# Kernel optimization log

Hardware: AMD Instinct MI355X
Metric: run time of the kernel (lower is better)

## Reference

```python
import jax, jax.numpy as jnp
import numpy as np

N = 50000      # nodes
E = 800000     # edges (avg degree 16)
D_IN = 64
D_H = 64


def setup_inputs() -> dict:
    key = jax.random.key(0)
    k = jax.random.split(key, 4)
    x = jax.random.normal(k[0], (N, D_IN), dtype=jnp.float32)
    edge_index = jax.random.randint(k[1], (2, E), 0, N, dtype=jnp.int64)
    W1 = jax.random.normal(k[2], (D_IN, D_H), dtype=jnp.float32) * (1.0 / np.sqrt(D_IN))
    b1 = jnp.zeros((D_H,), dtype=jnp.float32)
    W2 = jax.random.normal(k[3], (D_H, 1), dtype=jnp.float32) * (1.0 / np.sqrt(D_H))
    b2 = jnp.zeros((1,), dtype=jnp.float32)
    return {"x": x, "edge_index": edge_index, "W1": W1, "b1": b1, "W2": W2, "b2": b2}


def gcn_conv(x, src, dst, W, b):
    """PyG-style GCNConv: linear -> symmetric-normalized scatter-aggregate + bias.
    src/dst already include self-loops."""
    n = x.shape[0]
    h = x @ W                                                   # [N, Dout]
    deg = jax.ops.segment_sum(jnp.ones_like(dst, dtype=h.dtype), dst, num_segments=n)
    dinv_sqrt = jnp.where(deg > 0, jax.lax.rsqrt(jnp.maximum(deg, 1e-12)), 0.0)
    norm = dinv_sqrt[src] * dinv_sqrt[dst]                       # [E+N]
    agg = jax.ops.segment_sum(h[src] * norm[:, None], dst, num_segments=n)
    return agg + b


def reference(x, edge_index, W1, b1, W2, b2):
    n = x.shape[0]
    loops = jnp.arange(n, dtype=edge_index.dtype)
    src = jnp.concatenate([edge_index[0], loops])                # add self-loops
    dst = jnp.concatenate([edge_index[1], loops])
    h = jax.nn.relu(gcn_conv(x, src, dst, W1, b1))               # [N, D_H]
    out = gcn_conv(h, src, dst, W2, b2)                          # [N, 1]
    return out.squeeze(-1)                                       # [N]
```

## Files before the change

kernel.cpp:

```cpp
#include <hip/hip_runtime.h>

#define D 64
#define PW2 256
#define PSH2 8
#define EPB 4096

__global__ __launch_bounds__(256) void k_hist(const int* __restrict__ dst, int E,
                                              int* __restrict__ counts, int NP) {
    extern __shared__ int lh[];
    int t = threadIdx.x, b = blockIdx.x;
    for (int i = t; i < NP; i += 256) lh[i] = 0;
    __syncthreads();
    int base = b * EPB;
#pragma unroll
    for (int k = 0; k < EPB / 256; ++k) {
        int e = base + k * 256 + t;
        if (e < E) atomicAdd(&lh[dst[e] >> PSH2], 1);
    }
    __syncthreads();
    for (int i = t; i < NP; i += 256) counts[(size_t)b * NP + i] = lh[i];
}

__global__ __launch_bounds__(256) void k_scanA(int* __restrict__ counts, int NB, int NP,
                                               int* __restrict__ bin_total) {
    __shared__ int sh[256];
    int t = threadIdx.x, bin = blockIdx.x;
    int v = (t < NB) ? counts[(size_t)t * NP + bin] : 0;
    sh[t] = v;
    __syncthreads();
    for (int off = 1; off < 256; off <<= 1) {
        int u = (t >= off) ? sh[t - off] : 0;
        __syncthreads();
        sh[t] += u;
        __syncthreads();
    }
    if (t < NB) counts[(size_t)t * NP + bin] = sh[t] - v;
    if (t == 255) bin_total[bin] = sh[255];
}

__global__ __launch_bounds__(256) void k_scanB(const int* __restrict__ bin_total, int NP,
                                               int* __restrict__ bin_base) {
    __shared__ int sh[256];
    int t = threadIdx.x;
    int v = (t < NP) ? bin_total[t] : 0;
    sh[t] = v;
    __syncthreads();
    for (int off = 1; off < 256; off <<= 1) {
        int u = (t >= off) ? sh[t - off] : 0;
        __syncthreads();
        sh[t] += u;
        __syncthreads();
    }
    if (t < NP) bin_base[t] = sh[t] - v;
    if (t == 255) bin_base[NP] = sh[255];
}

__global__ __launch_bounds__(256) void k_scatter(const int* __restrict__ src,
        const int* __restrict__ dst, int E, const int* __restrict__ counts,
        const int* __restrict__ bin_base, int NP, int* __restrict__ csr_e) {
    extern __shared__ int cur[];
    int t = threadIdx.x, b = blockIdx.x;
    for (int i = t; i < NP; i += 256)
        cur[i] = counts[(size_t)b * NP + i] + bin_base[i];
    __syncthreads();
    int base = b * EPB;
#pragma unroll
    for (int k = 0; k < EPB / 256; ++k) {
        int e = base + k * 256 + t;
        if (e < E) {
            int s = src[e], d = dst[e];
            int pos = atomicAdd(&cur[d >> PSH2], 1);
            csr_e[pos] = s | ((d & (PW2 - 1)) << 16);
        }
    }
}

__global__ __launch_bounds__(256) void k_sort2(const int* __restrict__ csr_e,
        const int* __restrict__ bin_base, int n,
        int* __restrict__ csr_src, int* __restrict__ row_ptr,
        float* __restrict__ dinv) {
    __shared__ int cnt[PW2];
    __shared__ int sh[PW2];
    __shared__ int cursor[PW2];
    int t = threadIdx.x, p = blockIdx.x;
    cnt[t] = 0;
    __syncthreads();
    int beg = bin_base[p], end = bin_base[p + 1];
    for (int i = beg + t; i < end; i += 256) atomicAdd(&cnt[csr_e[i] >> 16], 1);
    __syncthreads();
    int val = cnt[t];
    sh[t] = val;
    __syncthreads();
    for (int off = 1; off < 256; off <<= 1) {
        int u = (t >= off) ? sh[t - off] : 0;
        __syncthreads();
        sh[t] += u;
        __syncthreads();
    }
    int excl = sh[t] - val;
    cursor[t] = beg + excl;
    int node = p * PW2 + t;
    if (node <= n) {
        row_ptr[node] = beg + excl;
        if (node < n) dinv[node] = rsqrtf((float)(val + 1));
    }
    __syncthreads();
    for (int i = beg + t; i < end; i += 256) {
        int e = csr_e[i];
        int q = atomicAdd(&cursor[e >> 16], 1);
        csr_src[q] = e & 0xFFFF;
    }
}

__global__ __launch_bounds__(256) void k_gather(
        const float* __restrict__ x, const float* __restrict__ dinv,
        const int* __restrict__ row_ptr, const int* __restrict__ csr_src,
        float* __restrict__ agg, int n) {
    int tid = threadIdx.x;
    int wave = tid >> 6, lane = tid & 63;
    int eg = lane >> 4, dg = lane & 15;
    int v = blockIdx.x * 4 + wave;
    if (v >= n) return;
    float dv = dinv[v];
    int beg = row_ptr[v], end = row_ptr[v + 1];

    float4 acc = make_float4(0.f, 0.f, 0.f, 0.f);
    if (eg == 0) {
        float4 xv = *(const float4*)&x[(size_t)v * D + dg * 4];
        float w = dv * dv;
        acc.x = xv.x * w; acc.y = xv.y * w; acc.z = xv.z * w; acc.w = xv.w * w;
    }
    int base = beg;
    for (; base + 16 <= end; base += 16) {
        int u0 = csr_src[base + eg];
        int u1 = csr_src[base + 4 + eg];
        int u2 = csr_src[base + 8 + eg];
        int u3 = csr_src[base + 12 + eg];
        float n0 = dinv[u0] * dv, n1 = dinv[u1] * dv;
        float n2 = dinv[u2] * dv, n3 = dinv[u3] * dv;
        float4 x0 = *(const float4*)&x[(size_t)u0 * D + dg * 4];
        float4 x1 = *(const float4*)&x[(size_t)u1 * D + dg * 4];
        float4 x2 = *(const float4*)&x[(size_t)u2 * D + dg * 4];
        float4 x3 = *(const float4*)&x[(size_t)u3 * D + dg * 4];
        acc.x = fmaf(x0.x, n0, acc.x); acc.y = fmaf(x0.y, n0, acc.y);
        acc.z = fmaf(x0.z, n0, acc.z); acc.w = fmaf(x0.w, n0, acc.w);
        acc.x = fmaf(x1.x, n1, acc.x); acc.y = fmaf(x1.y, n1, acc.y);
        acc.z = fmaf(x1.z, n1, acc.z); acc.w = fmaf(x1.w, n1, acc.w);
        acc.x = fmaf(x2.x, n2, acc.x); acc.y = fmaf(x2.y, n2, acc.y);
        acc.z = fmaf(x2.z, n2, acc.z); acc.w = fmaf(x2.w, n2, acc.w);
        acc.x = fmaf(x3.x, n3, acc.x); acc.y = fmaf(x3.y, n3, acc.y);
        acc.w = fmaf(x3.w, n3, acc.w); acc.z = fmaf(x3.z, n3, acc.z);
    }
    for (; base + 8 <= end; base += 8) {
        int u0 = csr_src[base + eg];
        int u1 = csr_src[base + 4 + eg];
        float n0 = dinv[u0] * dv, n1 = dinv[u1] * dv;
        float4 x0 = *(const float4*)&x[(size_t)u0 * D + dg * 4];
        float4 x1 = *(const float4*)&x[(size_t)u1 * D + dg * 4];
        acc.x = fmaf(x0.x, n0, acc.x); acc.y = fmaf(x0.y, n0, acc.y);
        acc.z = fmaf(x0.z, n0, acc.z); acc.w = fmaf(x0.w, n0, acc.w);
        acc.x = fmaf(x1.x, n1, acc.x); acc.y = fmaf(x1.y, n1, acc.y);
        acc.z = fmaf(x1.z, n1, acc.z); acc.w = fmaf(x1.w, n1, acc.w);
    }
    for (; base < end; base += 4) {
        int idx = base + eg;
        if (idx < end) {
            int u = csr_src[idx];
            float nrm = dinv[u] * dv;
            float4 xv = *(const float4*)&x[(size_t)u * D + dg * 4];
            acc.x = fmaf(xv.x, nrm, acc.x); acc.y = fmaf(xv.y, nrm, acc.y);
            acc.z = fmaf(xv.z, nrm, acc.z); acc.w = fmaf(xv.w, nrm, acc.w);
        }
    }
#pragma unroll
    for (int off = 16; off <= 32; off <<= 1) {
        acc.x += __shfl_xor(acc.x, off, 64);
        acc.y += __shfl_xor(acc.y, off, 64);
        acc.z += __shfl_xor(acc.z, off, 64);
        acc.w += __shfl_xor(acc.w, off, 64);
    }
    if (eg == 0) *(float4*)&agg[(size_t)v * D + dg * 4] = acc;
}

#define NPW 16
__global__ __launch_bounds__(256) void k_gemm(
        const float* __restrict__ agg, const float* __restrict__ dinv,
        const float* __restrict__ W1, const float* __restrict__ b1,
        const float* __restrict__ W2, float* __restrict__ sd, int n) {
    __shared__ float lrow[4][D];
    int tid = threadIdx.x;
    int wave = tid >> 6, lane = tid & 63;
    float w1c[D];
#pragma unroll
    for (int d = 0; d < D; ++d) w1c[d] = W1[d * D + lane];
    float b1l = b1[lane], w2l = W2[lane];
    int v0 = (blockIdx.x * 4 + wave) * NPW;
    for (int k = 0; k < NPW; ++k) {
        int v = v0 + k;
        if (v >= n) break;
        lrow[wave][lane] = agg[(size_t)v * D + lane];
        __builtin_amdgcn_wave_barrier();
        float h = b1l;
#pragma unroll
        for (int db = 0; db < D; db += 4) {
            float4 r = *(const float4*)&lrow[wave][db];
            h = fmaf(r.x, w1c[db], h);
            h = fmaf(r.y, w1c[db + 1], h);
            h = fmaf(r.z, w1c[db + 2], h);
            h = fmaf(r.w, w1c[db + 3], h);
        }
        float tt = fmaxf(h, 0.0f) * w2l;
#pragma unroll
        for (int off = 1; off <= 32; off <<= 1) tt += __shfl_xor(tt, off, 64);
        if (lane == 0) sd[v] = tt * dinv[v];
        __builtin_amdgcn_wave_barrier();
    }
}

__global__ __launch_bounds__(256) void k_out(const float* __restrict__ sd,
        const float* __restrict__ dinv, const int* __restrict__ row_ptr,
        const int* __restrict__ csr_src, const float* __restrict__ b2,
        float* __restrict__ out, int n) {
    int t = blockIdx.x * blockDim.x + threadIdx.x;
    int v = t >> 3, r = t & 7;
    if (v >= n) return;
    int beg = row_ptr[v], end = row_ptr[v + 1];
    float a = (r == 0) ? sd[v] : 0.0f;
    for (int i = beg + r; i < end; i += 8) a += sd[csr_src[i]];
    a += __shfl_xor(a, 1, 64);
    a += __shfl_xor(a, 2, 64);
    a += __shfl_xor(a, 4, 64);
    if (r == 0) out[v] = b2[0] + a * dinv[v];
}

extern "C" void kernel_launch(void* const* d_in, const int* in_sizes, int n_in,
                              void* d_out, int out_size, void* d_ws, size_t ws_size,
                              hipStream_t stream) {
    const float* x  = (const float*)d_in[0];
    const int*   ei = (const int*)d_in[1];
    const float* W1 = (const float*)d_in[2];
    const float* b1 = (const float*)d_in[3];
    const float* W2 = (const float*)d_in[4];
    const float* b2 = (const float*)d_in[5];

    int n = in_sizes[0] / D;
    int E = in_sizes[1] / 2;
    const int* src = ei;
    const int* dst = ei + E;

    int NP = (n + PW2 - 1) / PW2;
    int NB = (E + EPB - 1) / EPB;

    char* ws = (char*)d_ws;
    auto take = [&](size_t bytes) {
        char* p = ws;
        ws += (bytes + 255) & ~(size_t)255;
        return p;
    };
    int*   counts    = (int*)take((size_t)NB * NP * sizeof(int));
    int*   bin_total = (int*)take((size_t)NP * sizeof(int));
    int*   bin_base  = (int*)take((size_t)(NP + 1) * sizeof(int));
    int*   csr_e     = (int*)take((size_t)E * sizeof(int));
    int*   csr_src   = (int*)take((size_t)E * sizeof(int));
    int*   row_ptr   = (int*)take((size_t)(n + 1) * sizeof(int));
    float* dinv      = (float*)take((size_t)n * sizeof(float));
    float* sd        = (float*)take((size_t)n * sizeof(float));
    float* agg       = (float*)take((size_t)n * D * sizeof(float));

    float* out = (float*)d_out;
    size_t ldsNP = (size_t)NP * sizeof(int);

    k_hist<<<NB, 256, ldsNP, stream>>>(dst, E, counts, NP);
    k_scanA<<<NP, 256, 0, stream>>>(counts, NB, NP, bin_total);
    k_scanB<<<1, 256, 0, stream>>>(bin_total, NP, bin_base);
    k_scatter<<<NB, 256, ldsNP, stream>>>(src, dst, E, counts, bin_base, NP, csr_e);
    k_sort2<<<NP, 256, 0, stream>>>(csr_e, bin_base, n, csr_src, row_ptr, dinv);

    k_gather<<<(n + 3) / 4, 256, 0, stream>>>(x, dinv, row_ptr, csr_src, agg, n);
    k_gemm<<<(n + 4 * NPW - 1) / (4 * NPW), 256, 0, stream>>>(agg, dinv, W1, b1,
                                                              W2, sd, n);
    k_out<<<((size_t)n * 8 + 255) / 256, 256, 0, stream>>>(sd, dinv, row_ptr, csr_src,
                                                           b2, out, n);
}
```

Measured before the change: 92.39 us.

## Gather neighbor features from fp16 copy of x and fold bin scan into consumers

```diff
diff --git a/kernel.cpp b/kernel.cpp
--- a/kernel.cpp
+++ b/kernel.cpp
@@ -1,9 +1,20 @@
 #include <hip/hip_runtime.h>
+#include <hip/hip_fp16.h>
 
 #define D 64
 #define PW2 256
 #define PSH2 8
 #define EPB 4096
+
+__global__ void k_cast(const float4* __restrict__ x4, __half2* __restrict__ xh2,
+                       int total4) {
+    int i = blockIdx.x * blockDim.x + threadIdx.x;
+    if (i < total4) {
+        float4 v = x4[i];
+        xh2[2 * i]     = __floats2half2_rn(v.x, v.y);
+        xh2[2 * i + 1] = __floats2half2_rn(v.z, v.w);
+    }
+}
 
 __global__ __launch_bounds__(256) void k_hist(const int* __restrict__ dst, int E,
                                               int* __restrict__ counts, int NP) {
@@ -38,30 +49,22 @@
     if (t == 255) bin_total[bin] = sh[255];
 }
 
-__global__ __launch_bounds__(256) void k_scanB(const int* __restrict__ bin_total, int NP,
-                                               int* __restrict__ bin_base) {
-    __shared__ int sh[256];
-    int t = threadIdx.x;
-    int v = (t < NP) ? bin_total[t] : 0;
-    sh[t] = v;
-    __syncthreads();
-    for (int off = 1; off < 256; off <<= 1) {
-        int u = (t >= off) ? sh[t - off] : 0;
-        __syncthreads();
-        sh[t] += u;
-        __syncthreads();
-    }
-    if (t < NP) bin_base[t] = sh[t] - v;
-    if (t == 255) bin_base[NP] = sh[255];
-}
-
 __global__ __launch_bounds__(256) void k_scatter(const int* __restrict__ src,
         const int* __restrict__ dst, int E, const int* __restrict__ counts,
-        const int* __restrict__ bin_base, int NP, int* __restrict__ csr_e) {
+        const int* __restrict__ bin_total, int NP, int* __restrict__ csr_e) {
+    __shared__ int bs[256];
     extern __shared__ int cur[];
     int t = threadIdx.x, b = blockIdx.x;
-    for (int i = t; i < NP; i += 256)
-        cur[i] = counts[(size_t)b * NP + i] + bin_base[i];
+    int v = (t < NP) ? bin_total[t] : 0;
+    bs[t] = v;
+    __syncthreads();
+    for (int off = 1; off < 256; off <<= 1) {
+        int u = (t >= off) ? bs[t - off] : 0;
+        __syncthreads();
+        bs[t] += u;
+        __syncthreads();
+    }
+    if (t < NP) cur[t] = counts[(size_t)b * NP + t] + (bs[t] - v);
     __syncthreads();
     int base = b * EPB;
 #pragma unroll
@@ -76,16 +79,28 @@
 }
 
 __global__ __launch_bounds__(256) void k_sort2(const int* __restrict__ csr_e,
-        const int* __restrict__ bin_base, int n,
+        const int* __restrict__ bin_total, int NP, int n,
         int* __restrict__ csr_src, int* __restrict__ row_ptr,
         float* __restrict__ dinv) {
+    __shared__ int bs[256];
     __shared__ int cnt[PW2];
     __shared__ int sh[PW2];
     __shared__ int cursor[PW2];
+    __shared__ int s_beg, s_end;
     int t = threadIdx.x, p = blockIdx.x;
+    int bv = (t < NP) ? bin_total[t] : 0;
+    bs[t] = bv;
+    __syncthreads();
+    for (int off = 1; off < 256; off <<= 1) {
+        int u = (t >= off) ? bs[t - off] : 0;
+        __syncthreads();
+        bs[t] += u;
+        __syncthreads();
+    }
+    if (t == p) { s_beg = bs[t] - bv; s_end = bs[t]; }
     cnt[t] = 0;
     __syncthreads();
-    int beg = bin_base[p], end = bin_base[p + 1];
+    int beg = s_beg, end = s_end;
     for (int i = beg + t; i < end; i += 256) atomicAdd(&cnt[csr_e[i] >> 16], 1);
     __syncthreads();
     int val = cnt[t];
@@ -113,9 +128,9 @@
 }
 
 __global__ __launch_bounds__(256) void k_gather(
-        const float* __restrict__ x, const float* __restrict__ dinv,
-        const int* __restrict__ row_ptr, const int* __restrict__ csr_src,
-        float* __restrict__ agg, int n) {
+        const __half2* __restrict__ xh, const float* __restrict__ x,
+        const float* __restrict__ dinv, const int* __restrict__ row_ptr,
+        const int* __restrict__ csr_src, float* __restrict__ agg, int n) {
     int tid = threadIdx.x;
     int wave = tid >> 6, lane = tid & 63;
     int eg = lane >> 4, dg = lane & 15;
@@ -138,38 +153,48 @@
         int u3 = csr_src[base + 12 + eg];
         float n0 = dinv[u0] * dv, n1 = dinv[u1] * dv;
         float n2 = dinv[u2] * dv, n3 = dinv[u3] * dv;
-        float4 x0 = *(const float4*)&x[(size_t)u0 * D + dg * 4];
-        float4 x1 = *(const float4*)&x[(size_t)u1 * D + dg * 4];
-        float4 x2 = *(const float4*)&x[(size_t)u2 * D + dg * 4];
-        float4 x3 = *(const float4*)&x[(size_t)u3 * D + dg * 4];
-        acc.x = fmaf(x0.x, n0, acc.x); acc.y = fmaf(x0.y, n0, acc.y);
-        acc.z = fmaf(x0.z, n0, acc.z); acc.w = fmaf(x0.w, n0, acc.w);
-        acc.x = fmaf(x1.x, n1, acc.x); acc.y = fmaf(x1.y, n1, acc.y);
-        acc.z = fmaf(x1.z, n1, acc.z); acc.w = fmaf(x1.w, n1, acc.w);
-        acc.x = fmaf(x2.x, n2, acc.x); acc.y = fmaf(x2.y, n2, acc.y);
-        acc.z = fmaf(x2.z, n2, acc.z); acc.w = fmaf(x2.w, n2, acc.w);
-        acc.x = fmaf(x3.x, n3, acc.x); acc.y = fmaf(x3.y, n3, acc.y);
-        acc.w = fmaf(x3.w, n3, acc.w); acc.z = fmaf(x3.z, n3, acc.z);
+        const __half2* p0 = xh + (size_t)u0 * 32 + dg * 2;
+        const __half2* p1 = xh + (size_t)u1 * 32 + dg * 2;
+        const __half2* p2 = xh + (size_t)u2 * 32 + dg * 2;
+        const __half2* p3 = xh + (size_t)u3 * 32 + dg * 2;
+        __half2 a0 = p0[0], b0 = p0[1];
+        __half2 a1 = p1[0], b1 = p1[1];
+        __half2 a2 = p2[0], b2 = p2[1];
+        __half2 a3 = p3[0], b3 = p3[1];
+        float2 f;
+        f = __half22float2(a0); acc.x = fmaf(f.x, n0, acc.x); acc.y = fmaf(f.y, n0, acc.y);
+        f = __half22float2(b0); acc.z = fmaf(f.x, n0, acc.z); acc.w = fmaf(f.y, n0, acc.w);
+        f = __half22float2(a1); acc.x = fmaf(f.x, n1, acc.x); acc.y = fmaf(f.y, n1, acc.y);
+        f = __half22float2(b1); acc.z = fmaf(f.x, n1, acc.z); acc.w = fmaf(f.y, n1, acc.w);
+        f = __half22float2(a2); acc.x = fmaf(f.x, n2, acc.x); acc.y = fmaf(f.y, n2, acc.y);
+        f = __half22float2(b2); acc.z = fmaf(f.x, n2, acc.z); acc.w = fmaf(f.y, n2, acc.w);
+        f = __half22float2(a3); acc.x = fmaf(f.x, n3, acc.x); acc.y = fmaf(f.y, n3, acc.y);
+        f = __half22float2(b3); acc.z = fmaf(f.x, n3, acc.z); acc.w = fmaf(f.y, n3, acc.w);
     }
     for (; base + 8 <= end; base += 8) {
         int u0 = csr_src[base + eg];
         int u1 = csr_src[base + 4 + eg];
         float n0 = dinv[u0] * dv, n1 = dinv[u1] * dv;
-        float4 x0 = *(const float4*)&x[(size_t)u0 * D + dg * 4];
-        float4 x1 = *(const float4*)&x[(size_t)u1 * D + dg * 4];
-        acc.x = fmaf(x0.x, n0, acc.x); acc.y = fmaf(x0.y, n0, acc.y);
-        acc.z = fmaf(x0.z, n0, acc.z); acc.w = fmaf(x0.w, n0, acc.w);
-        acc.x = fmaf(x1.x, n1, acc.x); acc.y = fmaf(x1.y, n1, acc.y);
-        acc.z = fmaf(x1.z, n1, acc.z); acc.w = fmaf(x1.w, n1, acc.w);
+        const __half2* p0 = xh + (size_t)u0 * 32 + dg * 2;
+        const __half2* p1 = xh + (size_t)u1 * 32 + dg * 2;
+        __half2 a0 = p0[0], b0 = p0[1];
+        __half2 a1 = p1[0], b1 = p1[1];
+        float2 f;
+        f = __half22float2(a0); acc.x = fmaf(f.x, n0, acc.x); acc.y = fmaf(f.y, n0, acc.y);
+        f = __half22float2(b0); acc.z = fmaf(f.x, n0, acc.z); acc.w = fmaf(f.y, n0, acc.w);
+        f = __half22float2(a1); acc.x = fmaf(f.x, n1, acc.x); acc.y = fmaf(f.y, n1, acc.y);
+        f = __half22float2(b1); acc.z = fmaf(f.x, n1, acc.z); acc.w = fmaf(f.y, n1, acc.w);
     }
     for (; base < end; base += 4) {
         int idx = base + eg;
         if (idx < end) {
             int u = csr_src[idx];
             float nrm = dinv[u] * dv;
-            float4 xv = *(const float4*)&x[(size_t)u * D + dg * 4];
-            acc.x = fmaf(xv.x, nrm, acc.x); acc.y = fmaf(xv.y, nrm, acc.y);
-            acc.z = fmaf(xv.z, nrm, acc.z); acc.w = fmaf(xv.w, nrm, acc.w);
+            const __half2* p0 = xh + (size_t)u * 32 + dg * 2;
+            __half2 a0 = p0[0], b0 = p0[1];
+            float2 f;
+            f = __half22float2(a0); acc.x = fmaf(f.x, nrm, acc.x); acc.y = fmaf(f.y, nrm, acc.y);
+            f = __half22float2(b0); acc.z = fmaf(f.x, nrm, acc.z); acc.w = fmaf(f.y, nrm, acc.w);
         }
     }
 #pragma unroll
@@ -257,26 +282,28 @@
         ws += (bytes + 255) & ~(size_t)255;
         return p;
     };
-    int*   counts    = (int*)take((size_t)NB * NP * sizeof(int));
-    int*   bin_total = (int*)take((size_t)NP * sizeof(int));
-    int*   bin_base  = (int*)take((size_t)(NP + 1) * sizeof(int));
-    int*   csr_e     = (int*)take((size_t)E * sizeof(int));
-    int*   csr_src   = (int*)take((size_t)E * sizeof(int));
-    int*   row_ptr   = (int*)take((size_t)(n + 1) * sizeof(int));
-    float* dinv      = (float*)take((size_t)n * sizeof(float));
-    float* sd        = (float*)take((size_t)n * sizeof(float));
-    float* agg       = (float*)take((size_t)n * D * sizeof(float));
+    int*     counts    = (int*)take((size_t)NB * NP * sizeof(int));
+    int*     bin_total = (int*)take((size_t)NP * sizeof(int));
+    int*     csr_e     = (int*)take((size_t)E * sizeof(int));
+    int*     csr_src   = (int*)take((size_t)E * sizeof(int));
+    int*     row_ptr   = (int*)take((size_t)(n + 1) * sizeof(int));
+    float*   dinv      = (float*)take((size_t)n * sizeof(float));
+    float*   sd        = (float*)take((size_t)n * sizeof(float));
+    float*   agg       = (float*)take((size_t)n * D * sizeof(float));
+    __half2* xh        = (__half2*)take((size_t)n * D * sizeof(__half));
 
     float* out = (float*)d_out;
     size_t ldsNP = (size_t)NP * sizeof(int);
 
+    int total4 = n * D / 4;
+    k_cast<<<(total4 + 255) / 256, 256, 0, stream>>>((const float4*)x, xh, total4);
+
     k_hist<<<NB, 256, ldsNP, stream>>>(dst, E, counts, NP);
     k_scanA<<<NP, 256, 0, stream>>>(counts, NB, NP, bin_total);
-    k_scanB<<<1, 256, 0, stream>>>(bin_total, NP, bin_base);
-    k_scatter<<<NB, 256, ldsNP, stream>>>(src, dst, E, counts, bin_base, NP, csr_e);
-    k_sort2<<<NP, 256, 0, stream>>>(csr_e, bin_base, n, csr_src, row_ptr, dinv);
-
-    k_gather<<<(n + 3) / 4, 256, 0, stream>>>(x, dinv, row_ptr, csr_src, agg, n);
+    k_scatter<<<NB, 256, ldsNP, stream>>>(src, dst, E, counts, bin_total, NP, csr_e);
+    k_sort2<<<NP, 256, 0, stream>>>(csr_e, bin_total, NP, n, csr_src, row_ptr, dinv);
+
+    k_gather<<<(n + 3) / 4, 256, 0, stream>>>(xh, x, dinv, row_ptr, csr_src, agg, n);
     k_gemm<<<(n + 4 * NPW - 1) / (4 * NPW), 256, 0, stream>>>(agg, dinv, W1, b1,
                                                               W2, sd, n);
     k_out<<<((size_t)n * 8 + 255) / 256, 256, 0, stream>>>(sd, dinv, row_ptr, csr_src,
```

Result: no change. 93.60 us (+1.3%).
